# Kernel tuning notes

Hardware: AMD Instinct MI355X
Metric: run time of the kernel (lower is better)

The kernel has to match this reference:

```python
import jax, jax.numpy as jnp
import numpy as np
from jax import lax

T, N, H, L, NL, C, NA = 256, 1024, 256, 16, 32, 64, 16


def setup_inputs():
    ks = jax.random.split(jax.random.key(0), 20)
    g = lambda i, shape, s=0.05: jax.random.normal(ks[i], shape, jnp.float32) * s
    return dict(
        condition=jax.random.normal(ks[0], (T, N, C), jnp.float32),
        active=jax.random.randint(ks[1], (T, N), 0, L),
        lines=jax.random.randint(ks[2], (N, L), 0, NL),
        actions=jax.random.randint(ks[3], (T, N), 0, NA),
        h0=g(4, (N, H), 1.0), p0=g(5, (N, 1), 1.0), pp0=g(6, (N, 2), 1.0),
        embed=g(7, (NL, H)),
        wih_f=g(8, (3 * H, H)), whh_f=g(9, (3 * H, H)),
        bih_f=jnp.zeros(3 * H), bhh_f=jnp.zeros(3 * H),
        wih_b=g(10, (3 * H, H)), whh_b=g(11, (3 * H, H)),
        bih_b=jnp.zeros(3 * H), bhh_b=jnp.zeros(3 * H),
        f_w0=g(12, (H, C + 2 * H)), f_b0=jnp.zeros(H),
        f_w1=g(13, (H, H)), f_b1=jnp.zeros(H),
        f_w2=g(14, (H, H)), f_b2=jnp.zeros(H),
        c_wih=g(15, (3 * H, H)), c_whh=g(16, (3 * H, H)),
        c_bih=jnp.zeros(3 * H), c_bhh=jnp.zeros(3 * H),
        w_critic=g(17, (1, H)), b_critic=jnp.zeros(1),
        w_actor=g(18, (NA, H)), b_actor=jnp.zeros(NA),
    )


def _gru_step(h, x, wih, whh, bih, bhh):
    # PyTorch GRU/GRUCell gate order: r, z, n
    gi = x @ wih.T + bih
    gh = h @ whh.T + bhh
    ir, iz, inn = jnp.split(gi, 3, -1)
    hr, hz, hn = jnp.split(gh, 3, -1)
    r = jax.nn.sigmoid(ir + hr)
    z = jax.nn.sigmoid(iz + hz)
    n = jnp.tanh(inn + r * hn)
    return (1.0 - z) * n + z * h


def reference(condition, active, lines, actions, h0, p0, pp0, embed,
              wih_f, whh_f, bih_f, bhh_f, wih_b, whh_b, bih_b, bhh_b,
              f_w0, f_b0, f_w1, f_b1, f_w2, f_b2,
              c_wih, c_whh, c_bih, c_bhh, w_critic, b_critic, w_actor, b_actor):
    Tn, Nn, _ = condition.shape
    Ln = lines.shape[1]
    Hh = h0.shape[1]
    # ---- task encoder: bidirectional GRU over every cyclic roll of the line embeddings ----
    M = embed[lines]                                   # [N, L, H]
    seq = jnp.transpose(M, (1, 0, 2))                  # [L, N, H]
    idx = (jnp.arange(Ln)[:, None] + jnp.arange(Ln)[None, :]) % Ln  # roll -i: idx[i,j]=(i+j)%L
    X = seq[idx]                                       # [roll, t, N, H]
    X = jnp.transpose(X, (1, 0, 2, 3)).reshape(Ln, Ln * Nn, Hh)  # seq-first, rolls folded into batch
    z0 = jnp.zeros((Ln * Nn, Hh), condition.dtype)
    h_f, _ = lax.scan(lambda h, x: (_gru_step(h, x, wih_f, whh_f, bih_f, bhh_f), None), z0, X)
    h_b, _ = lax.scan(lambda h, x: (_gru_step(h, x, wih_b, whh_b, bih_b, bhh_b), None), z0, X[::-1])
    Hmem = jnp.concatenate([h_f.reshape(Ln, Nn, Hh), h_b.reshape(Ln, Nn, Hh)], -1)  # [L, N, 2H]

    def mlp(x):
        x = jax.nn.relu(x @ f_w0.T + f_b0)
        x = jax.nn.relu(x @ f_w1.T + f_b1)
        return jax.nn.relu(x @ f_w2.T + f_b2)

    Ridx = jnp.arange(Nn)

    def step(h, xs):
        cond_t, w_t, a_t = xs
        r = Hmem[w_t, Ridx]                            # gather H[w, R] -> [N, 2H]
        h = _gru_step(h, mlp(jnp.concatenate([cond_t, r], -1)), c_wih, c_whh, c_bih, c_bhh)
        probs = jax.nn.softmax(h @ w_actor.T + b_actor)
        v = h @ w_critic.T + b_critic
        return h, (a_t, w_t, v, h, probs)

    _, (a_s, w_s, v_s, h_s, ap_s) = lax.scan(step, h0, (condition, active, actions))
    fdt = condition.dtype
    p_s = jnp.broadcast_to(p0[None], (Tn,) + p0.shape)
    pp_s = jnp.broadcast_to(pp0[None], (Tn,) + pp0.shape)
    # packed RecurrentState field order: a, p, w, v, h, a_probs, p_probs
    return jnp.concatenate([a_s[..., None].astype(fdt), p_s,
                            w_s[..., None].astype(fdt), v_s,
                            h_s, ap_s, pp_s], -1)      # [T, N, 4 + H + NA + 2]
```

## Files before the change

kernel.cpp:

```cpp
#include <hip/hip_runtime.h>
#include <stdint.h>

#define DI __device__ __forceinline__

typedef __attribute__((ext_vector_type(8))) short short8;
typedef __attribute__((ext_vector_type(4))) float f32x4;

DI float bf2f(uint16_t u){ union{uint32_t i; float f;} v; v.i = ((uint32_t)u)<<16; return v.f; }
DI uint16_t f2bf(float f){
    union{float f; uint32_t i;} v; v.f = f;
    uint32_t r = v.i + 0x7FFFu + ((v.i>>16)&1u);
    return (uint16_t)(r>>16);
}
DI float sigm(float x){ return 1.f/(1.f+__expf(-x)); }
DI float tanhx(float x){ float e=__expf(-2.f*fabsf(x)); float t=(1.f-e)/(1.f+e); return x<0.f? -t : t; }
DI void unp2(uint32_t u, float&a, float&b){ a = bf2f((uint16_t)(u&0xFFFFu)); b = bf2f((uint16_t)(u>>16)); }

#define MFMA(a,b,c) __builtin_amdgcn_mfma_f32_16x16x32_bf16((a),(b),(c),0,0,0)


__global__ void k_detect(const uint16_t* __restrict__ embed, int* __restrict__ flag){
  __shared__ int bad;
  if (threadIdx.x == 0) bad = 0;
  __syncthreads();
  float v = bf2f(embed[threadIdx.x]);
  if (!(fabsf(v) <= 100.f)) atomicAdd(&bad, 1);
  __syncthreads();
  if (threadIdx.x == 0) flag[0] = (bad > 0) ? 1 : 0;
}

struct CvtEnt { const void* src; uint16_t* dst; int n; int pad; };
struct CvtTab { CvtEnt e[26]; };

__global__ __launch_bounds__(1024) void k_convert_small(CvtTab tab, const int* __restrict__ flag){
  CvtEnt E = tab.e[blockIdx.x];
  if (flag[0]){
    const float* s = (const float*)E.src;
    for (int i = threadIdx.x; i < E.n; i += 1024) E.dst[i] = f2bf(s[i]);
  } else {
    const uint16_t* s = (const uint16_t*)E.src;
    for (int i = threadIdx.x; i < E.n; i += 1024) E.dst[i] = s[i];
  }
}

__global__ __launch_bounds__(256) void k_convert_big(const void* __restrict__ src,
                                                     uint16_t* __restrict__ dst,
                                                     int n8, const int* __restrict__ flag){
  int i = blockIdx.x*256 + threadIdx.x;
  if (i >= n8) return;
  if (flag[0]){
    const float4* s = (const float4*)src;
    float4 a = s[(size_t)i*2], b = s[(size_t)i*2+1];
    union { uint16_t u[8]; uint4 v; } o;
    o.u[0]=f2bf(a.x); o.u[1]=f2bf(a.y); o.u[2]=f2bf(a.z); o.u[3]=f2bf(a.w);
    o.u[4]=f2bf(b.x); o.u[5]=f2bf(b.y); o.u[6]=f2bf(b.z); o.u[7]=f2bf(b.w);
    *(uint4*)&dst[(size_t)i*8] = o.v;
  } else {
    *(uint4*)&dst[(size_t)i*8] = ((const uint4*)src)[i];
  }
}

__global__ __launch_bounds__(256) void k_tables(
    const uint16_t* __restrict__ embed,
    const uint16_t* __restrict__ wih_f, const uint16_t* __restrict__ bih_f,
    const uint16_t* __restrict__ wih_b, const uint16_t* __restrict__ bih_b,
    float* __restrict__ GiE)
{
  int dir = blockIdx.x >> 5, e = blockIdx.x & 31;
  const uint16_t* wih = dir ? wih_b : wih_f;
  const uint16_t* bih = dir ? bih_b : bih_f;
  __shared__ float emb[256];
  int tid = threadIdx.x;
  emb[tid] = bf2f(embed[e*256 + tid]);
  __syncthreads();
  for (int c = tid; c < 768; c += 256){
    float s = bf2f(bih[c]);
    const uint32_t* wr = (const uint32_t*)(wih + (size_t)c*256);
    #pragma unroll 4
    for (int k2 = 0; k2 < 128; ++k2){
      float a, b; unp2(wr[k2], a, b);
      s += emb[k2*2]*a + emb[k2*2+1]*b;
    }
    GiE[(size_t)(dir*32 + e)*768 + c] = s;
  }
}

__global__ __launch_bounds__(512,2) void k_encoder(
    const int* __restrict__ lines, const float* __restrict__ GiE,
    const uint16_t* __restrict__ whh_f, const uint16_t* __restrict__ whh_b,
    const uint16_t* __restrict__ bhh_f, const uint16_t* __restrict__ bhh_b,
    uint16_t* __restrict__ Hmem )
{
  int b = blockIdx.x;
  int dir = b >> 8; b &= 255;
  int r = b >> 4, n0 = (b & 15) << 6;
  const uint16_t* whh = dir ? whh_b : whh_f;
  const uint16_t* bhh = dir ? bhh_b : bhh_f;
  const float* gte = GiE + (size_t)dir * (32*768);

  __shared__ uint16_t hbuf[64*264];
  __shared__ int lid_s[64*16];

  int tid = threadIdx.x;
  for (int s = tid; s < 1024; s += 512) lid_s[s] = lines[(n0 + (s>>4))*16 + (s&15)];
  for (int s = tid; s < 8448; s += 512) ((uint32_t*)hbuf)[s] = 0u;

  int w = tid >> 6, lane = tid & 63, l15 = lane & 15, q = lane >> 4;
  int cw = w << 5;
  int nc[6];
  nc[0]=cw; nc[1]=cw+16; nc[2]=256+cw; nc[3]=256+cw+16; nc[4]=512+cw; nc[5]=512+cw+16;
  float bh[6];
  #pragma unroll
  for (int i=0;i<6;i++) bh[i] = bf2f(bhh[nc[i]+l15]);

  float hreg[4][2][4];
  #pragma unroll
  for (int a=0;a<4;a++)
    #pragma unroll
    for (int c=0;c<2;c++)
      #pragma unroll
      for (int e=0;e<4;e++) hreg[a][c][e]=0.f;

  __syncthreads();

  for (int j=0;j<16;++j){
    int jj = dir ? (15-j) : j;
    int pos = (r + jj) & 15;
    f32x4 acc[4][6];
    #pragma unroll
    for (int mt=0;mt<4;mt++)
      #pragma unroll
      for (int u=0;u<6;u++) acc[mt][u] = (f32x4){0.f,0.f,0.f,0.f};
    #pragma unroll
    for (int kb=0;kb<8;kb++){
      short8 af[4];
      #pragma unroll
      for (int mt=0;mt<4;mt++)
        af[mt] = *(const short8*)&hbuf[(mt*16+l15)*264 + kb*32 + q*8];
      #pragma unroll
      for (int u=0;u<6;u++){
        short8 bf = *(const short8*)&whh[(size_t)(nc[u]+l15)*256 + kb*32 + q*8];
        #pragma unroll
        for (int mt=0;mt<4;mt++) acc[mt][u] = MFMA(af[mt], bf, acc[mt][u]);
      }
    }
    __syncthreads();
    #pragma unroll
    for (int mt=0;mt<4;mt++){
      int lidv[4];
      #pragma unroll
      for (int e=0;e<4;e++) lidv[e] = lid_s[(mt*16 + q*4 + e)*16 + pos];
      float gv[4][6];
      #pragma unroll
      for (int e=0;e<4;e++)
        #pragma unroll
        for (int u=0;u<6;u++) gv[e][u] = gte[(size_t)lidv[e]*768 + nc[u] + l15];
      #pragma unroll
      for (int c=0;c<2;c++)
        #pragma unroll
        for (int e=0;e<4;e++){
          float ghr = acc[mt][c  ][e] + bh[c  ];
          float ghz = acc[mt][2+c][e] + bh[2+c];
          float ghn = acc[mt][4+c][e] + bh[4+c];
          float rr = sigm(gv[e][c] + ghr);
          float zz = sigm(gv[e][2+c] + ghz);
          float nn = tanhx(gv[e][4+c] + rr*ghn);
          float hn = (1.f-zz)*nn + zz*hreg[mt][c][e];
          hreg[mt][c][e] = hn;
          hbuf[(mt*16 + q*4 + e)*264 + cw + c*16 + l15] = f2bf(hn);
        }
    }
    __syncthreads();
  }
  for (int s = tid; s < 8192; s += 512){
    int row = s >> 7, cp = (s & 127) << 1;
    uint32_t v = *(uint32_t*)&hbuf[row*264 + cp];
    *(uint32_t*)&Hmem[(size_t)((r<<10) + n0 + row)*512 + (dir<<8) + cp] = v;
  }
}

__global__ __launch_bounds__(256,3) void k_gemm(
    const uint16_t* __restrict__ A, int lda,
    const uint16_t* __restrict__ W, int ldw, int woff,
    const uint16_t* __restrict__ bias,
    const int* __restrict__ gidx, const uint16_t* __restrict__ G,
    uint16_t* __restrict__ C, int ldc, int K, int flags)
{
  int n0 = blockIdx.x << 6, m0 = blockIdx.y << 7;
  int tid = threadIdx.x, w = tid>>6, lane = tid&63, l15 = lane&15, q = lane>>4;
  __shared__ uint16_t As[128*56];
  __shared__ uint16_t Ws[64*56];
  f32x4 acc[2][4];
  #pragma unroll
  for (int mt=0;mt<2;mt++)
    #pragma unroll
    for (int nt=0;nt<4;nt++) acc[mt][nt]=(f32x4){0.f,0.f,0.f,0.f};
  int nk = K >> 5;
  int arow0 = tid >> 2, ach = (tid & 3) << 3;
  for (int kb = 0; kb < nk; ++kb){
    int k0 = kb << 5;
    *(uint4*)&As[arow0*56 + ach]      = *(const uint4*)&A[(size_t)(m0+arow0)*lda + k0 + ach];
    *(uint4*)&As[(arow0+64)*56 + ach] = *(const uint4*)&A[(size_t)(m0+arow0+64)*lda + k0 + ach];
    *(uint4*)&Ws[arow0*56 + ach]      = *(const uint4*)&W[(size_t)(n0+arow0)*ldw + woff + k0 + ach];
    __syncthreads();
    short8 af[2], bfr[4];
    #pragma unroll
    for (int mt=0;mt<2;mt++) af[mt] = *(const short8*)&As[(w*32 + mt*16 + l15)*56 + q*8];
    #pragma unroll
    for (int nt=0;nt<4;nt++) bfr[nt] = *(const short8*)&Ws[(nt*16 + l15)*56 + q*8];
    #pragma unroll
    for (int mt=0;mt<2;mt++)
      #pragma unroll
      for (int nt=0;nt<4;nt++) acc[mt][nt] = MFMA(af[mt], bfr[nt], acc[mt][nt]);
    __syncthreads();
  }
  float bv[4] = {0.f,0.f,0.f,0.f};
  if (flags & 2){
    #pragma unroll
    for (int nt=0;nt<4;nt++) bv[nt] = bf2f(bias[n0 + nt*16 + l15]);
  }
  if (flags & 8){
    #pragma unroll
    for (int mt=0;mt<2;mt++)
      #pragma unroll
      for (int nt=0;nt<4;nt++){
        int row0 = m0 + w*32 + mt*16 + q*4;
        int t = row0 >> 10, n = row0 & 1023;
        int nblk = n >> 4;
        int colv = n0 + nt*16 + l15;
        int wp = (colv >> 5) & 7, u = (colv >> 8)*2 + ((colv >> 4) & 1);
        size_t base = ((((size_t)t*64 + nblk)*8 + wp)*16 + (size_t)l15)*96
                      + (size_t)q*24 + (size_t)u*4;
        union { uint16_t us[4]; uint2 v; } o;
        #pragma unroll
        for (int e=0;e<4;e++) o.us[e] = f2bf(acc[mt][nt][e] + bv[nt]);
        *(uint2*)&C[base] = o.v;
      }
  } else {
    #pragma unroll
    for (int mt=0;mt<2;mt++)
      #pragma unroll
      for (int e=0;e<4;e++){
        int row = m0 + w*32 + mt*16 + q*4 + e;
        size_t gb = 0;
        if (flags & 4) gb = ((size_t)gidx[row]*1024 + (size_t)(row & 1023))*256;
        #pragma unroll
        for (int nt=0;nt<4;nt++){
          int col = n0 + nt*16 + l15;
          float v = acc[mt][nt][e] + bv[nt];
          if (flags & 4) v += bf2f(G[gb + col]);
          if (flags & 1) v = fmaxf(v, 0.f);
          C[(size_t)row*ldc + col] = f2bf(v);
        }
      }
  }
}

__global__ __launch_bounds__(512,1) void k_phasec(
    const uint16_t* __restrict__ Gi, const uint16_t* __restrict__ c_whh,
    const uint16_t* __restrict__ c_bhh, const uint16_t* __restrict__ hinit,
    uint16_t* __restrict__ hcur, uint16_t* __restrict__ h_s, int Tc)
{
  int bx = blockIdx.x;
  int n0 = bx << 4;
  int tid = threadIdx.x, w = tid>>6, lane = tid&63, l15 = lane&15, q = lane>>4;
  int cw = w<<5;
  int nc[6];
  nc[0]=cw; nc[1]=cw+16; nc[2]=256+cw; nc[3]=256+cw+16; nc[4]=512+cw; nc[5]=512+cw+16;

  __shared__ uint16_t hb[2][16*264];

  const size_t gstep = (size_t)64*8*16*96;
  size_t goff0 = (((size_t)bx*8 + w)*16 + (size_t)l15)*96 + (size_t)q*24;

  for (int s = tid; s < 2048; s += 512){
    int row = s >> 7, cp = (s&127) << 1;
    uint32_t v = *(const uint32_t*)&hinit[(size_t)(n0+row)*256 + cp];
    *(uint32_t*)&hb[0][row*264 + cp] = v;
  }
  float bh[6];
  #pragma unroll
  for (int i=0;i<6;i++) bh[i] = bf2f(c_bhh[nc[i]+l15]);
  float hreg[2][4];
  #pragma unroll
  for (int c=0;c<2;c++)
    #pragma unroll
    for (int e=0;e<4;e++)
      hreg[c][e] = bf2f(hinit[(size_t)(n0+q*4+e)*256 + cw + c*16 + l15]);
  short8 bw[8][6];
  #pragma unroll
  for (int kb=0;kb<8;kb++)
    #pragma unroll
    for (int u=0;u<6;u++)
      bw[kb][u] = *(const short8*)&c_whh[(size_t)(nc[u]+l15)*256 + kb*32 + q*8];
  short8 gpk[3];
  {
    const uint16_t* gb = Gi + goff0;
    gpk[0] = *(const short8*)&gb[0];
    gpk[1] = *(const short8*)&gb[8];
    gpk[2] = *(const short8*)&gb[16];
  }
  __syncthreads();

#define GV(u,e) bf2f((uint16_t)gpk[((u)*4+(e))>>3][((u)*4+(e))&7])

  int p = 0;
  for (int t=0;t<Tc;++t){
    if (t > 0){
      #pragma unroll
      for (int i=0;i<4;i++){
        int s = tid + i*512;
        int row = s >> 7, cp = (s&127) << 1;
        *(uint32_t*)&h_s[(size_t)(((t-1)<<10) + n0 + row)*256 + cp] =
            *(const uint32_t*)&hb[p][row*264 + cp];
      }
    }
    f32x4 acc[6];
    #pragma unroll
    for (int u=0;u<6;u++) acc[u] = (f32x4){0.f,0.f,0.f,0.f};
    #pragma unroll
    for (int kb=0;kb<8;kb++){
      short8 af = *(const short8*)&hb[p][l15*264 + kb*32 + q*8];
      #pragma unroll
      for (int u=0;u<6;u++)
        acc[u] = MFMA(af, bw[kb][u], acc[u]);
    }
    #pragma unroll
    for (int c=0;c<2;c++)
      #pragma unroll
      for (int e=0;e<4;e++){
        int row = q*4+e;
        float ghr = acc[c  ][e]+bh[c  ];
        float ghz = acc[2+c][e]+bh[2+c];
        float ghn = acc[4+c][e]+bh[4+c];
        float rr = sigm(GV(c,e)+ghr), zz = sigm(GV(2+c,e)+ghz);
        float nn = tanhx(GV(4+c,e) + rr*ghn);
        float hn = (1.f-zz)*nn + zz*hreg[c][e];
        hreg[c][e] = hn;
        hb[p^1][row*264 + cw + c*16 + l15] = f2bf(hn);
      }
    {
      int tn = (t+1 < Tc) ? (t+1) : t;
      const uint16_t* gb = Gi + (size_t)tn*gstep + goff0;
      gpk[0] = *(const short8*)&gb[0];
      gpk[1] = *(const short8*)&gb[8];
      gpk[2] = *(const short8*)&gb[16];
    }
    __syncthreads();
    p ^= 1;
  }
#undef GV
  for (int s = tid; s < 2048; s += 512){
    int row = s >> 7, cp = (s&127) << 1;
    uint32_t v = *(uint32_t*)&hb[p][row*264 + cp];
    *(uint32_t*)&hcur[(size_t)(n0+row)*256 + cp] = v;
    *(uint32_t*)&h_s[(size_t)(((Tc-1)<<10) + n0 + row)*256 + cp] = v;
  }
}

__global__ __launch_bounds__(256) void k_phased(
    const uint16_t* __restrict__ h_s ,
    const uint16_t* __restrict__ w_actor, const uint16_t* __restrict__ b_actor,
    const uint16_t* __restrict__ w_critic, const uint16_t* __restrict__ b_critic,
    const int* __restrict__ actions , const int* __restrict__ active,
    const uint16_t* __restrict__ p0, const uint16_t* __restrict__ pp0,
    void* __restrict__ out, const int* __restrict__ flag, int row0g)
{
  int r0 = blockIdx.x << 6;
  __shared__ uint16_t hb[64*264];
  __shared__ uint16_t wa[17*256];
  __shared__ float lv[64*18];
  int tid = threadIdx.x;
  for (int s = tid; s < 2048; s += 256){
    int row = s >> 5, ch = (s & 31) << 3;
    *(uint4*)&hb[row*264 + ch] = *(const uint4*)&h_s[(size_t)(r0+row)*256 + ch];
  }
  for (int s = tid; s < 512; s += 256)
    *(uint4*)&wa[s*8] = *(const uint4*)&w_actor[s*8];
  if (tid < 32) *(uint4*)&wa[4096 + tid*8] = *(const uint4*)&w_critic[tid*8];
  __syncthreads();
  int row = tid & 63, cg = tid >> 6;
  for (int c = cg; c < 17; c += 4){
    const uint32_t* hr = (const uint32_t*)&hb[row*264];
    const uint32_t* wr = (const uint32_t*)&wa[c*256];
    float s = 0.f;
    #pragma unroll 4
    for (int k2=0;k2<128;k2++){
      float a,b,c2,d; unp2(hr[k2],a,b); unp2(wr[k2],c2,d);
      s += a*c2 + b*d;
    }
    s += (c<16) ? bf2f(b_actor[c]) : bf2f(b_critic[0]);
    lv[row*18 + c] = s;
  }
  __syncthreads();
  if (tid < 64){
    float mx = -1e30f;
    #pragma unroll
    for (int c=0;c<16;c++) mx = fmaxf(mx, lv[tid*18+c]);
    float sum = 0.f;
    #pragma unroll
    for (int c=0;c<16;c++){ float ev = __expf(lv[tid*18+c]-mx); lv[tid*18+c]=ev; sum+=ev; }
    float inv = 1.f/sum;
    #pragma unroll
    for (int c=0;c<16;c++) lv[tid*18+c] *= inv;
  }
  __syncthreads();
  int isf = flag[0];
  float* outf = (float*)out;
  uint16_t* outb = (uint16_t*)out;
  for (int s = tid; s < 64*278; s += 256){
    int rw = s / 278, c = s - rw*278;
    int gr = row0g + r0 + rw;
    int n  = (r0 + rw) & 1023;
    float fv;
    if (c >= 4 && c < 260)        fv = bf2f(hb[rw*264 + (c-4)]);
    else if (c >= 260 && c < 276) fv = lv[rw*18 + (c-260)];
    else if (c == 0)              fv = (float)actions[gr];
    else if (c == 1)              fv = bf2f(p0[n]);
    else if (c == 2)              fv = (float)active[gr];
    else if (c == 3)              fv = lv[rw*18+16];
    else                          fv = bf2f(pp0[(n<<1) + (c-276)]);
    size_t off = (size_t)gr*278 + c;
    if (isf) outf[off] = fv;
    else     outb[off] = f2bf(fv);
  }
}

extern "C" void kernel_launch(void* const* d_in, const int* in_sizes, int n_in,
                              void* d_out, int out_size, void* d_ws, size_t ws_size,
                              hipStream_t stream)
{
  (void)in_sizes; (void)n_in; (void)out_size;
  const int* active  = (const int*)d_in[1];
  const int* lines   = (const int*)d_in[2];
  const int* actions = (const int*)d_in[3];

  char* wsb = (char*)d_ws;
  size_t off = 0;
  auto aln  = [](size_t x){ return (x + 255) & ~(size_t)255; };
  auto carve = [&](size_t bytes)->char*{ char* p = wsb + off; off += aln(bytes); return p; };

  int*      flag   = (int*)     carve(256);
  float*    GiE    = (float*)   carve((size_t)2*32*768*4);
  uint16_t* Hmem   = (uint16_t*)carve((size_t)16*1024*512*2);
  uint16_t* Rpart  = (uint16_t*)carve((size_t)16384*256*2);
  uint16_t* hcur   = (uint16_t*)carve((size_t)1024*256*2);
  uint16_t* condbf = (uint16_t*)carve((size_t)262144*64*2);

  struct Item { int idx; int n; };
  const Item items[26] = {
    {8,196608},{9,196608},{10,768},{11,768},{12,196608},{13,196608},{14,768},{15,768},
    {16,147456},{17,256},{18,65536},{19,256},{20,65536},{21,256},
    {22,196608},{23,196608},{24,768},{25,768},
    {26,256},{27,1},{28,4096},{29,16},{5,1024},{6,2048},{7,8192},{4,262144}};
  uint16_t* bf[30] = {};
  CvtTab tab;
  for (int i=0;i<26;i++){
    uint16_t* d = (uint16_t*)carve((size_t)items[i].n*2);
    bf[items[i].idx] = d;
    tab.e[i].src = d_in[items[i].idx];
    tab.e[i].dst = d;
    tab.e[i].n   = items[i].n;
    tab.e[i].pad = 0;
  }

  size_t fixedBytes = off;
  int Tc = 4;
  const int cands[7] = {256,128,64,32,16,8,4};
  for (int i=0;i<7;i++){
    int c = cands[i];
    size_t need = fixedBytes + 2*aln((size_t)c*1024*256*2) + aln((size_t)c*1024*768*2);
    if (need <= ws_size){ Tc = c; break; }
  }
  uint16_t* Xa  = (uint16_t*)carve((size_t)Tc*1024*256*2);
  uint16_t* Xb  = (uint16_t*)carve((size_t)Tc*1024*256*2);
  uint16_t* Gic = (uint16_t*)carve((size_t)Tc*1024*768*2);

  k_detect<<<1,256,0,stream>>>((const uint16_t*)d_in[7], flag);
  k_convert_small<<<26,1024,0,stream>>>(tab, flag);
  k_convert_big<<<8192,256,0,stream>>>(d_in[0], condbf, 2097152, flag);

  k_tables<<<64,256,0,stream>>>(bf[7], bf[8], bf[10], bf[12], bf[14], GiE);
  k_encoder<<<512,512,0,stream>>>(lines, GiE, bf[9], bf[13], bf[11], bf[15], Hmem);
  k_gemm<<<dim3(4,128),256,0,stream>>>(Hmem,512, bf[16],576,64, nullptr, nullptr,nullptr,
                                       Rpart,256, 512, 0);
  for (int t0 = 0; t0 < 256; t0 += Tc){
    const uint16_t* condc = condbf + (size_t)t0*1024*64;
    const int* activec = active + t0*1024;
    k_gemm<<<dim3(4,Tc*8),256,0,stream>>>(condc,64, bf[16],576,0, bf[17], activec, Rpart,
                                          Xa,256, 64, 7);
    k_gemm<<<dim3(4,Tc*8),256,0,stream>>>(Xa,256, bf[18],256,0, bf[19], nullptr,nullptr,
                                          Xb,256, 256, 3);
    k_gemm<<<dim3(4,Tc*8),256,0,stream>>>(Xb,256, bf[20],256,0, bf[21], nullptr,nullptr,
                                          Xa,256, 256, 3);
    k_gemm<<<dim3(12,Tc*8),256,0,stream>>>(Xa,256, bf[22],256,0, bf[24], nullptr,nullptr,
                                           Gic,768, 256, 10);
    k_phasec<<<64,512,0,stream>>>(Gic, bf[23], bf[25], (t0==0 ? bf[4] : hcur), hcur, Xb, Tc);
    k_phased<<<Tc*16,256,0,stream>>>(Xb, bf[28], bf[29], bf[26], bf[27],
                                     actions, active, bf[5], bf[6],
                                     d_out, flag, t0*1024);
  }
}
```

Before: 2.933 ms.

## Split recurrent GRU kernel across 16 waves per block with repacked gate-input layout

The sequential GRU recurrence kernel now runs 1024 threads (16 waves) per block instead of 512, with each wave owning one 16-column tile per gate instead of two. This halves the MFMA chain and gate math per wave on the serial critical path. The GEMM epilogue that writes gate inputs is rewritten to a matching packed layout, and the next-step gate-input prefetch is issued before the MFMAs to hide its latency. The cost is more waves contending for LDS and barriers per step, and the (1024,4) launch bound may limit registers, since the recurrent weights stay held in registers.

Result: slower. 3.419 ms (+16.6%).

```diff
diff --git a/kernel.cpp b/kernel.cpp
--- a/kernel.cpp
+++ b/kernel.cpp
@@ -226,11 +226,11 @@
       for (int nt=0;nt<4;nt++){
         int row0 = m0 + w*32 + mt*16 + q*4;
         int t = row0 >> 10, n = row0 & 1023;
-        int nblk = n >> 4;
+        int nblk = n >> 4, qp = (n & 15) >> 2;
         int colv = n0 + nt*16 + l15;
-        int wp = (colv >> 5) & 7, u = (colv >> 8)*2 + ((colv >> 4) & 1);
-        size_t base = ((((size_t)t*64 + nblk)*8 + wp)*16 + (size_t)l15)*96
-                      + (size_t)q*24 + (size_t)u*4;
+        int u = colv >> 8, wp = (colv >> 4) & 15, lp = colv & 15;
+        size_t base = ((((size_t)t*64 + nblk)*16 + wp)*16 + (size_t)lp)*48
+                      + (size_t)qp*12 + (size_t)u*4;
         union { uint16_t us[4]; uint2 v; } o;
         #pragma unroll
         for (int e=0;e<4;e++) o.us[e] = f2bf(acc[mt][nt][e] + bv[nt]);
@@ -256,7 +256,7 @@
   }
 }
 
-__global__ __launch_bounds__(512,1) void k_phasec(
+__global__ __launch_bounds__(1024,4) void k_phasec(
     const uint16_t* __restrict__ Gi, const uint16_t* __restrict__ c_whh,
     const uint16_t* __restrict__ c_bhh, const uint16_t* __restrict__ hinit,
     uint16_t* __restrict__ hcur, uint16_t* __restrict__ h_s, int Tc)
@@ -264,93 +264,90 @@
   int bx = blockIdx.x;
   int n0 = bx << 4;
   int tid = threadIdx.x, w = tid>>6, lane = tid&63, l15 = lane&15, q = lane>>4;
-  int cw = w<<5;
-  int nc[6];
-  nc[0]=cw; nc[1]=cw+16; nc[2]=256+cw; nc[3]=256+cw+16; nc[4]=512+cw; nc[5]=512+cw+16;
+  int c0 = w << 4;
+  int nc[3]; nc[0]=c0; nc[1]=256+c0; nc[2]=512+c0;
 
   __shared__ uint16_t hb[2][16*264];
 
-  const size_t gstep = (size_t)64*8*16*96;
-  size_t goff0 = (((size_t)bx*8 + w)*16 + (size_t)l15)*96 + (size_t)q*24;
-
-  for (int s = tid; s < 2048; s += 512){
+  const size_t gstep = (size_t)1024*768;
+  size_t goff0 = (((size_t)bx*16 + w)*16 + (size_t)l15)*48 + (size_t)q*12;
+
+  for (int s = tid; s < 2048; s += 1024){
     int row = s >> 7, cp = (s&127) << 1;
-    uint32_t v = *(const uint32_t*)&hinit[(size_t)(n0+row)*256 + cp];
-    *(uint32_t*)&hb[0][row*264 + cp] = v;
-  }
-  float bh[6];
+    *(uint32_t*)&hb[0][row*264 + cp] = *(const uint32_t*)&hinit[(size_t)(n0+row)*256 + cp];
+  }
+  float bh[3];
   #pragma unroll
-  for (int i=0;i<6;i++) bh[i] = bf2f(c_bhh[nc[i]+l15]);
-  float hreg[2][4];
+  for (int u=0;u<3;u++) bh[u] = bf2f(c_bhh[nc[u]+l15]);
+  float hreg[4];
   #pragma unroll
-  for (int c=0;c<2;c++)
-    #pragma unroll
-    for (int e=0;e<4;e++)
-      hreg[c][e] = bf2f(hinit[(size_t)(n0+q*4+e)*256 + cw + c*16 + l15]);
-  short8 bw[8][6];
+  for (int e=0;e<4;e++)
+    hreg[e] = bf2f(hinit[(size_t)(n0+q*4+e)*256 + c0 + l15]);
+  short8 bw[8][3];
   #pragma unroll
   for (int kb=0;kb<8;kb++)
     #pragma unroll
-    for (int u=0;u<6;u++)
+    for (int u=0;u<3;u++)
       bw[kb][u] = *(const short8*)&c_whh[(size_t)(nc[u]+l15)*256 + kb*32 + q*8];
-  short8 gpk[3];
+  uint2 gpk[3];
   {
     const uint16_t* gb = Gi + goff0;
-    gpk[0] = *(const short8*)&gb[0];
-    gpk[1] = *(const short8*)&gb[8];
-    gpk[2] = *(const short8*)&gb[16];
-  }
-  __syncthreads();
-
-#define GV(u,e) bf2f((uint16_t)gpk[((u)*4+(e))>>3][((u)*4+(e))&7])
+    gpk[0] = *(const uint2*)&gb[0];
+    gpk[1] = *(const uint2*)&gb[4];
+    gpk[2] = *(const uint2*)&gb[8];
+  }
+  __syncthreads();
+
+#define GV(u,e) bf2f((uint16_t)((((u)*4+(e))&1) ? \
+    (((((u)*4+(e))&2) ? gpk[(u)].y : gpk[(u)].x) >> 16) : \
+    (((((u)*4+(e))&2) ? gpk[(u)].y : gpk[(u)].x) & 0xFFFFu)))
 
   int p = 0;
   for (int t=0;t<Tc;++t){
     if (t > 0){
       #pragma unroll
-      for (int i=0;i<4;i++){
-        int s = tid + i*512;
+      for (int i=0;i<2;i++){
+        int s = tid + i*1024;
         int row = s >> 7, cp = (s&127) << 1;
         *(uint32_t*)&h_s[(size_t)(((t-1)<<10) + n0 + row)*256 + cp] =
             *(const uint32_t*)&hb[p][row*264 + cp];
       }
     }
-    f32x4 acc[6];
-    #pragma unroll
-    for (int u=0;u<6;u++) acc[u] = (f32x4){0.f,0.f,0.f,0.f};
-    #pragma unroll
-    for (int kb=0;kb<8;kb++){
-      short8 af = *(const short8*)&hb[p][l15*264 + kb*32 + q*8];
-      #pragma unroll
-      for (int u=0;u<6;u++)
-        acc[u] = MFMA(af, bw[kb][u], acc[u]);
-    }
-    #pragma unroll
-    for (int c=0;c<2;c++)
-      #pragma unroll
-      for (int e=0;e<4;e++){
-        int row = q*4+e;
-        float ghr = acc[c  ][e]+bh[c  ];
-        float ghz = acc[2+c][e]+bh[2+c];
-        float ghn = acc[4+c][e]+bh[4+c];
-        float rr = sigm(GV(c,e)+ghr), zz = sigm(GV(2+c,e)+ghz);
-        float nn = tanhx(GV(4+c,e) + rr*ghn);
-        float hn = (1.f-zz)*nn + zz*hreg[c][e];
-        hreg[c][e] = hn;
-        hb[p^1][row*264 + cw + c*16 + l15] = f2bf(hn);
-      }
+    uint2 gnx0, gnx1, gnx2;
     {
       int tn = (t+1 < Tc) ? (t+1) : t;
       const uint16_t* gb = Gi + (size_t)tn*gstep + goff0;
-      gpk[0] = *(const short8*)&gb[0];
-      gpk[1] = *(const short8*)&gb[8];
-      gpk[2] = *(const short8*)&gb[16];
-    }
+      gnx0 = *(const uint2*)&gb[0];
+      gnx1 = *(const uint2*)&gb[4];
+      gnx2 = *(const uint2*)&gb[8];
+    }
+    f32x4 acc[3];
+    #pragma unroll
+    for (int u=0;u<3;u++) acc[u] = (f32x4){0.f,0.f,0.f,0.f};
+    #pragma unroll
+    for (int kb=0;kb<8;kb++){
+      short8 af = *(const short8*)&hb[p][l15*264 + kb*32 + q*8];
+      #pragma unroll
+      for (int u=0;u<3;u++)
+        acc[u] = MFMA(af, bw[kb][u], acc[u]);
+    }
+    #pragma unroll
+    for (int e=0;e<4;e++){
+      float ghr = acc[0][e]+bh[0];
+      float ghz = acc[1][e]+bh[1];
+      float ghn = acc[2][e]+bh[2];
+      float rr = sigm(GV(0,e)+ghr), zz = sigm(GV(1,e)+ghz);
+      float nn = tanhx(GV(2,e) + rr*ghn);
+      float hn = (1.f-zz)*nn + zz*hreg[e];
+      hreg[e] = hn;
+      hb[p^1][(q*4+e)*264 + c0 + l15] = f2bf(hn);
+    }
+    gpk[0] = gnx0; gpk[1] = gnx1; gpk[2] = gnx2;
     __syncthreads();
     p ^= 1;
   }
 #undef GV
-  for (int s = tid; s < 2048; s += 512){
+  for (int s = tid; s < 2048; s += 1024){
     int row = s >> 7, cp = (s&127) << 1;
     uint32_t v = *(uint32_t*)&hb[p][row*264 + cp];
     *(uint32_t*)&hcur[(size_t)(n0+row)*256 + cp] = v;
@@ -495,7 +492,7 @@
                                           Xa,256, 256, 3);
     k_gemm<<<dim3(12,Tc*8),256,0,stream>>>(Xa,256, bf[22],256,0, bf[24], nullptr,nullptr,
                                            Gic,768, 256, 10);
-    k_phasec<<<64,512,0,stream>>>(Gic, bf[23], bf[25], (t0==0 ? bf[4] : hcur), hcur, Xb, Tc);
+    k_phasec<<<64,1024,0,stream>>>(Gic, bf[23], bf[25], (t0==0 ? bf[4] : hcur), hcur, Xb, Tc);
     k_phased<<<Tc*16,256,0,stream>>>(Xb, bf[28], bf[29], bf[26], bf[27],
                                      actions, active, bf[5], bf[6],
                                      d_out, flag, t0*1024);
```
